# Performance work log

Hardware: AMD Instinct MI355X
Metric: run time of the kernel (lower is better)

## Reference

```python
import jax, jax.numpy as jnp
import numpy as np

B, N, D, H = 32, 64, 256, 256
WORD_NUM, REL_NUM, POS_NUM, CAT_NUM = 50000, 50, 48, 5


def setup_inputs() -> dict:
    key = jax.random.key(0)
    ks = jax.random.split(key, 20)
    rng = np.random.default_rng(0)
    # valid dependency trees: head[i] < i, head[0] = -1 (root)
    heads_np = np.zeros((B, N), dtype=np.int32)
    for b in range(B):
        heads_np[b, 0] = -1
        for i in range(1, N):
            heads_np[b, i] = rng.integers(0, i)
    p = lambda k, shape: (0.02 * jax.random.normal(k, shape)).astype(jnp.float32)
    z = lambda shape: jnp.zeros(shape, jnp.float32)
    return {
        "xs": jax.random.randint(ks[0], (B, N), 0, WORD_NUM),
        "heads": jnp.asarray(heads_np),
        "rels": jax.random.randint(ks[1], (B, N), 0, REL_NUM),
        "labels": jax.random.randint(ks[2], (B, N), 0, WORD_NUM),
        "poss": jax.random.randint(ks[3], (B, N), 0, POS_NUM),
        "xlengths": jnp.full((B,), N, dtype=jnp.int32),
        "target_start": jnp.zeros((B,), jnp.int32),
        "target_end": jnp.full((B,), N - 1, jnp.int32),
        "x_mask": jnp.ones((B, N), jnp.float32),
        # parameters
        "emb_W": p(ks[4], (WORD_NUM, D)),
        "rel_W": p(ks[5], (REL_NUM, D)),
        "gru_Wi_f": p(ks[6], (2 * D, 3 * H)), "gru_Wh_f": p(ks[7], (H, 3 * H)),
        "gru_bi_f": z((3 * H,)), "gru_bh_f": z((3 * H,)),
        "gru_Wi_b": p(ks[8], (2 * D, 3 * H)), "gru_Wh_b": p(ks[9], (H, 3 * H)),
        "gru_bi_b": z((3 * H,)), "gru_bh_b": z((3 * H,)),
        "Wt": p(ks[10], (2 * H, D)), "bt": z((D,)),
        "dt_Wx": p(ks[11], (2 * D, 3 * H)), "dt_Uh": p(ks[12], (H, 3 * H)), "dt_b": z((3 * H,)),
        "td_Wx": p(ks[13], (2 * D, 3 * H)), "td_Uh": p(ks[14], (H, 3 * H)), "td_b": z((3 * H,)),
        "fc_W": p(ks[15], (2 * H, 100)), "fc_b": z((100,)),
        "fc2_W": p(ks[16], (100, CAT_NUM)), "fc2_b": z((CAT_NUM,)),
    }


def _gru_cell(xpt, hprev, Uh, bh):
    gh = hprev @ Uh + bh
    xr, xz, xn = jnp.split(xpt, 3, axis=-1)
    hr, hz, hn = jnp.split(gh, 3, axis=-1)
    r = jax.nn.sigmoid(xr + hr)
    zg = jax.nn.sigmoid(xz + hz)
    n = jnp.tanh(xn + r * hn)
    return (1.0 - zg) * n + zg * hprev


def _gru_dir(x, Wi, Wh, bi, bh):
    # x: [B,N,2D] -> hidden sequence [B,N,H]
    xp = x @ Wi + bi  # precompute input projections
    def step(h, xpt):
        hnew = _gru_cell(xpt, h, Wh, bh)
        return hnew, hnew
    h0 = jnp.zeros((x.shape[0], Wh.shape[0]), x.dtype)
    _, hs = jax.lax.scan(step, h0, jnp.swapaxes(xp, 0, 1))
    return jnp.swapaxes(hs, 0, 1)


def _dt_tree(inputs, heads, Wx, Uh, b):
    # bottom-up (child-sum) tree GRU; heads[b,i] < i so reversed order is topological
    Bn, Nn, _ = inputs.shape
    Hh = Uh.shape[0]
    xp = inputs @ Wx + b
    bar = jnp.arange(Bn)
    def step(carry, idx):
        C, Hout = carry  # C: accumulated child hidden sums [B,N,H]
        h = _gru_cell(xp[:, idx], C[:, idx], Uh, jnp.zeros((3 * Hh,), inputs.dtype))
        Hout = Hout.at[:, idx].set(h)
        par = heads[:, idx]
        valid = par >= 0
        C = C.at[bar, jnp.where(valid, par, 0)].add(jnp.where(valid[:, None], h, 0.0))
        return (C, Hout), None
    H0 = jnp.zeros((Bn, Nn, Hh), inputs.dtype)
    (_, Hout), _ = jax.lax.scan(step, (H0, H0), jnp.arange(Nn - 1, -1, -1))
    return Hout


def _td_tree(inputs, heads, Wx, Uh, b):
    # top-down tree GRU: parent hidden flows to children; index order 0..N-1 is topological
    Bn, Nn, _ = inputs.shape
    Hh = Uh.shape[0]
    xp = inputs @ Wx + b
    bar = jnp.arange(Bn)
    def step(Hout, idx):
        par = heads[:, idx]
        valid = par >= 0
        hp = jnp.where(valid[:, None], Hout[bar, jnp.where(valid, par, 0)], 0.0)
        h = _gru_cell(xp[:, idx], hp, Uh, jnp.zeros((3 * Hh,), inputs.dtype))
        Hout = Hout.at[:, idx].set(h)
        return Hout, None
    H0 = jnp.zeros((Bn, Nn, Hh), inputs.dtype)
    Hout, _ = jax.lax.scan(step, H0, jnp.arange(Nn))
    return Hout


def reference(xs, heads, rels, labels, poss, xlengths, target_start, target_end, x_mask,
              emb_W, rel_W,
              gru_Wi_f, gru_Wh_f, gru_bi_f, gru_bh_f,
              gru_Wi_b, gru_Wh_b, gru_bi_b, gru_bh_b,
              Wt, bt, dt_Wx, dt_Uh, dt_b, td_Wx, td_Uh, td_b,
              fc_W, fc_b, fc2_W, fc2_b):
    word_emb = emb_W[xs]
    label_emb = emb_W[labels]  # original uses self.embedding for labels too
    emb = jnp.concatenate([word_emb, label_emb], axis=-1)  # [B,N,2D]
    fwd = _gru_dir(emb, gru_Wi_f, gru_Wh_f, gru_bi_f, gru_bh_f)
    bwd = jnp.flip(_gru_dir(jnp.flip(emb, 1), gru_Wi_b, gru_Wh_b, gru_bi_b, gru_bh_b), 1)
    grus = jnp.concatenate([fwd, bwd], axis=-1) @ Wt + bt  # transform -> [B,N,D]
    rel_emb = rel_W[rels]
    outputs = jnp.concatenate([grus, rel_emb], axis=-1)  # [B,N,2D]
    dt_out = _dt_tree(outputs, heads, dt_Wx, dt_Uh, dt_b)
    td_out = _td_tree(outputs, heads, td_Wx, td_Uh, td_b)
    ctx = jnp.concatenate([dt_out, td_out], axis=-1)  # [B,N,2H]
    ctx = jnp.max(ctx, axis=1)  # max_pool1d over length -> [B,2H]
    ctx = ctx @ fc_W + fc_b
    ctx = ctx @ fc2_W + fc2_b
    return ctx
```

## Files before the change

### kernel.cpp

```cpp
#include <hip/hip_runtime.h>


typedef _Float16 half2v __attribute__((ext_vector_type(2)));
typedef _Float16 half8 __attribute__((ext_vector_type(8)));
typedef unsigned int u32x32 __attribute__((ext_vector_type(32)));
typedef float f32x4v __attribute__((ext_vector_type(4)));

__device__ __forceinline__ float fdot2f(unsigned a, unsigned b, float c) {
#if __has_builtin(__builtin_amdgcn_fdot2)
  return __builtin_amdgcn_fdot2(__builtin_bit_cast(half2v, a),
                                __builtin_bit_cast(half2v, b), c, false);
#else
  half2v av = __builtin_bit_cast(half2v, a), bv = __builtin_bit_cast(half2v, b);
  return c + (float)av.x * (float)bv.x + (float)av.y * (float)bv.y;
#endif
}

__device__ __forceinline__ unsigned packh2(float x, float y) {
  half2v p;
  p.x = (_Float16)x;
  p.y = (_Float16)y;
  return __builtin_bit_cast(unsigned, p);
}
__device__ __forceinline__ float sigm(float x) { return 1.f / (1.f + __expf(-x)); }
__device__ __forceinline__ float tanh_fast(float x) {
  float cx = fminf(fmaxf(x, -15.f), 15.f);
  float e = __expf(2.f * cx);
  return (e - 1.f) / (e + 1.f);
}

__global__ __launch_bounds__(256) void pack_w(const float* __restrict__ W0,
                                              const float* __restrict__ W1,
                                              const float* __restrict__ W2,
                                              const float* __restrict__ W3, unsigned* P0,
                                              unsigned* P1, unsigned* P2, unsigned* P3) {
  const float* W;
  unsigned* P;
  switch (blockIdx.y) {
    case 0: W = W0; P = P0; break;
    case 1: W = W1; P = P1; break;
    case 2: W = W2; P = P2; break;
    default: W = W3; P = P3; break;
  }
  const int tid = blockIdx.x * 256 + threadIdx.x;
  const int i = tid & 3;
  const int u4 = tid >> 2;
  const int jg = u4 & 127;
  const int d4q = u4 >> 7;
  const int d4 = d4q % 48;
  const int q2 = d4q / 48;
  const int col2 = d4 / 24;
  const int rr = d4 % 24;
  const int g = rr >> 3;
  const int p4 = rr & 7;
  const int kp = p4 * 4 + i;
  const int k = q2 * 64 + kp * 2;
  const int col = g * 256 + col2 * 128 + jg;
  P[tid] = packh2(W[(size_t)k * 768 + col], W[(size_t)(k + 1) * 768 + col]);
}

template <int NP>
__device__ __forceinline__ void stage_w(const uint4* __restrict__ P4, int q2, int jg,
                                        int t, uint2 (*Wl)[512], u32x32& w0, u32x32& w1,
                                        u32x32& w2) {
#pragma unroll
  for (int p4 = 0; p4 < 8; ++p4) {
    uint4 v0 = P4[(q2 * 48 + p4) * 128 + jg];
    w0[4 * p4 + 0] = v0.x; w0[4 * p4 + 1] = v0.y;
    w0[4 * p4 + 2] = v0.z; w0[4 * p4 + 3] = v0.w;
    uint4 v1 = P4[(q2 * 48 + 8 + p4) * 128 + jg];
    w1[4 * p4 + 0] = v1.x; w1[4 * p4 + 1] = v1.y;
    w1[4 * p4 + 2] = v1.z; w1[4 * p4 + 3] = v1.w;
    uint4 v2 = P4[(q2 * 48 + 16 + p4) * 128 + jg];
    w2[4 * p4 + 0] = v2.x; w2[4 * p4 + 1] = v2.y;
    w2[4 * p4 + 2] = v2.z; w2[4 * p4 + 3] = v2.w;
  }
#pragma unroll
  for (int g = 0; g < 3; ++g)
#pragma unroll
    for (int p4 = 0; p4 < NP; ++p4) {
      uint4 v = P4[(q2 * 48 + 24 + g * 8 + p4) * 128 + jg];
      Wl[(g * NP + p4) * 2 + 0][t] = make_uint2(v.x, v.y);
      Wl[(g * NP + p4) * 2 + 1][t] = make_uint2(v.z, v.w);
    }
}

template <int NP>
__device__ __forceinline__ void dot_step(const u32x32& w0, const u32x32& w1,
                                         const u32x32& w2, const uint2 (*Wl)[512], int t,
                                         const uint4* __restrict__ P4, int sb,
                                         const uint4* hv4, float& a0, float& a1,
                                         float& a2, float& a3, float& a4, float& a5) {
#pragma unroll
  for (int c = 0; c < 8; ++c) {
    uint4 hu = hv4[c];
    a0 = fdot2f(w0[4 * c + 0], hu.x, a0); a0 = fdot2f(w0[4 * c + 1], hu.y, a0);
    a0 = fdot2f(w0[4 * c + 2], hu.z, a0); a0 = fdot2f(w0[4 * c + 3], hu.w, a0);
    a1 = fdot2f(w1[4 * c + 0], hu.x, a1); a1 = fdot2f(w1[4 * c + 1], hu.y, a1);
    a1 = fdot2f(w1[4 * c + 2], hu.z, a1); a1 = fdot2f(w1[4 * c + 3], hu.w, a1);
    a2 = fdot2f(w2[4 * c + 0], hu.x, a2); a2 = fdot2f(w2[4 * c + 1], hu.y, a2);
    a2 = fdot2f(w2[4 * c + 2], hu.z, a2); a2 = fdot2f(w2[4 * c + 3], hu.w, a2);
    if (c < NP) {
      uint2 u0 = Wl[(0 * NP + c) * 2 + 0][t], u1 = Wl[(0 * NP + c) * 2 + 1][t];
      a3 = fdot2f(u0.x, hu.x, a3); a3 = fdot2f(u0.y, hu.y, a3);
      a3 = fdot2f(u1.x, hu.z, a3); a3 = fdot2f(u1.y, hu.w, a3);
      uint2 v0 = Wl[(1 * NP + c) * 2 + 0][t], v1 = Wl[(1 * NP + c) * 2 + 1][t];
      a4 = fdot2f(v0.x, hu.x, a4); a4 = fdot2f(v0.y, hu.y, a4);
      a4 = fdot2f(v1.x, hu.z, a4); a4 = fdot2f(v1.y, hu.w, a4);
      uint2 x0 = Wl[(2 * NP + c) * 2 + 0][t], x1 = Wl[(2 * NP + c) * 2 + 1][t];
      a5 = fdot2f(x0.x, hu.x, a5); a5 = fdot2f(x0.y, hu.y, a5);
      a5 = fdot2f(x1.x, hu.z, a5); a5 = fdot2f(x1.y, hu.w, a5);
    } else {
      uint4 s0 = P4[sb + (0 * 8 + c) * 128];
      a3 = fdot2f(s0.x, hu.x, a3); a3 = fdot2f(s0.y, hu.y, a3);
      a3 = fdot2f(s0.z, hu.z, a3); a3 = fdot2f(s0.w, hu.w, a3);
      uint4 s1 = P4[sb + (1 * 8 + c) * 128];
      a4 = fdot2f(s1.x, hu.x, a4); a4 = fdot2f(s1.y, hu.y, a4);
      a4 = fdot2f(s1.z, hu.z, a4); a4 = fdot2f(s1.w, hu.w, a4);
      uint4 s2 = P4[sb + (2 * 8 + c) * 128];
      a5 = fdot2f(s2.x, hu.x, a5); a5 = fdot2f(s2.y, hu.y, a5);
      a5 = fdot2f(s2.z, hu.z, a5); a5 = fdot2f(s2.w, hu.w, a5);
    }
  }
}

__global__ void gather_emb(const int* __restrict__ xs, const int* __restrict__ labels,
                           const float* __restrict__ embW, float* __restrict__ emb) {
  const int row = blockIdx.x;
  const int t = threadIdx.x;
  const float4* W4 = (const float4*)embW;
  float4* dst = (float4*)(emb + (size_t)row * 512);
  if (t < 64)
    dst[t] = W4[(size_t)xs[row] * 64 + t];
  else
    dst[t] = W4[(size_t)labels[row] * 64 + (t - 64)];
}

__global__ void gather_rel(const int* __restrict__ rels, const float* __restrict__ relW,
                           float* __restrict__ outputs) {
  const int row = blockIdx.x;
  const int t = threadIdx.x;
  const float4* W4 = (const float4*)relW;
  float4* dst = (float4*)(outputs + (size_t)row * 512 + 256);
  dst[t] = W4[(size_t)rels[row] * 64 + t];
}

__global__ __launch_bounds__(256) void mm16s(const float* __restrict__ A,
                                             const float* __restrict__ W,
                                             const float* __restrict__ bias,
                                             float* __restrict__ C, int N, int ldc) {
  __shared__ __align__(16) _Float16 Ahi[64][40], Alo[64][40];
  __shared__ __align__(16) _Float16 Bhi[64][40], Blo[64][40];
  const int t = threadIdx.x, l = t & 63, w = t >> 6;
  const int bm = blockIdx.y * 64, bn = blockIdx.x * 64;
  const int ar = t >> 2, ac8 = (t & 3) * 8;
  const int bk = t >> 3, bn8 = (t & 7) * 8;
  f32x4v ac0 = {0.f, 0.f, 0.f, 0.f}, ac1 = ac0, ac2 = ac0, ac3 = ac0;
  const int fr = w * 16 + (l & 15), fc = (l >> 4) * 8, lo16 = l & 15;
  for (int kt = 0; kt < 512; kt += 32) {
    {
      const float* ap = A + (size_t)(bm + ar) * 512 + kt + ac8;
      float4 v0 = *(const float4*)ap;
      float4 v1 = *(const float4*)(ap + 4);
      float av[8] = {v0.x, v0.y, v0.z, v0.w, v1.x, v1.y, v1.z, v1.w};
#pragma unroll
      for (int i = 0; i < 8; ++i) {
        _Float16 h = (_Float16)av[i];
        Ahi[ar][ac8 + i] = h;
        Alo[ar][ac8 + i] = (_Float16)(av[i] - (float)h);
      }
    }
    {
      const float* wp = W + (size_t)(kt + bk) * N + bn + bn8;
      float4 v0 = *(const float4*)wp;
      float4 v1 = *(const float4*)(wp + 4);
      float wv[8] = {v0.x, v0.y, v0.z, v0.w, v1.x, v1.y, v1.z, v1.w};
#pragma unroll
      for (int i = 0; i < 8; ++i) {
        _Float16 h = (_Float16)wv[i];
        Bhi[bn8 + i][bk] = h;
        Blo[bn8 + i][bk] = (_Float16)(wv[i] - (float)h);
      }
    }
    __syncthreads();
    half8 avh = __builtin_bit_cast(half8, *(const uint4*)(&Ahi[fr][fc]));
    half8 avl = __builtin_bit_cast(half8, *(const uint4*)(&Alo[fr][fc]));
#define BH(NT) __builtin_bit_cast(half8, *(const uint4*)(&Bhi[(NT)*16 + lo16][fc]))
#define BL(NT) __builtin_bit_cast(half8, *(const uint4*)(&Blo[(NT)*16 + lo16][fc]))
    half8 b0h = BH(0), b1h = BH(1), b2h = BH(2), b3h = BH(3);
    half8 b0l = BL(0), b1l = BL(1), b2l = BL(2), b3l = BL(3);
#undef BH
#undef BL
    ac0 = __builtin_amdgcn_mfma_f32_16x16x32_f16(avh, b0h, ac0, 0, 0, 0);
    ac1 = __builtin_amdgcn_mfma_f32_16x16x32_f16(avh, b1h, ac1, 0, 0, 0);
    ac2 = __builtin_amdgcn_mfma_f32_16x16x32_f16(avh, b2h, ac2, 0, 0, 0);
    ac3 = __builtin_amdgcn_mfma_f32_16x16x32_f16(avh, b3h, ac3, 0, 0, 0);
    ac0 = __builtin_amdgcn_mfma_f32_16x16x32_f16(avh, b0l, ac0, 0, 0, 0);
    ac1 = __builtin_amdgcn_mfma_f32_16x16x32_f16(avh, b1l, ac1, 0, 0, 0);
    ac2 = __builtin_amdgcn_mfma_f32_16x16x32_f16(avh, b2l, ac2, 0, 0, 0);
    ac3 = __builtin_amdgcn_mfma_f32_16x16x32_f16(avh, b3l, ac3, 0, 0, 0);
    ac0 = __builtin_amdgcn_mfma_f32_16x16x32_f16(avl, b0h, ac0, 0, 0, 0);
    ac1 = __builtin_amdgcn_mfma_f32_16x16x32_f16(avl, b1h, ac1, 0, 0, 0);
    ac2 = __builtin_amdgcn_mfma_f32_16x16x32_f16(avl, b2h, ac2, 0, 0, 0);
    ac3 = __builtin_amdgcn_mfma_f32_16x16x32_f16(avl, b3h, ac3, 0, 0, 0);
    __syncthreads();
  }
  const int hi4 = l >> 4;
#define EPI(AC, NT)                                                            \
  {                                                                            \
    _Pragma("unroll") for (int i = 0; i < 4; ++i) {                            \
      const int row = bm + w * 16 + hi4 * 4 + i;                               \
      const int col = bn + (NT)*16 + lo16;                                     \
      C[(size_t)row * ldc + col] = (AC)[i] + bias[col];                        \
    }                                                                          \
  }
  EPI(ac0, 0) EPI(ac1, 1) EPI(ac2, 2) EPI(ac3, 3)
#undef EPI
}

__global__ __launch_bounds__(512) void gru_scan_h(
    const unsigned* __restrict__ Pf, const unsigned* __restrict__ Pb,
    const float* __restrict__ bh_f, const float* __restrict__ bh_b,
    const float* __restrict__ xp_f, const float* __restrict__ xp_b,
    float* __restrict__ grus) {
  const int b = blockIdx.x & 31, dir = blockIdx.x >> 5;
  const uint4* __restrict__ P4 = (const uint4*)(dir ? Pb : Pf);
  const float* __restrict__ bh = dir ? bh_b : bh_f;
  const float* __restrict__ xp = dir ? xp_b : xp_f;

  __shared__ uint2 Wl[36][512];
  __shared__ float part[4][3][256];
  __shared__ __align__(16) unsigned h2[128];

  const int t = threadIdx.x, jg = t & 127, q2 = t >> 7;
  const int sb = (q2 * 48 + 24) * 128 + jg;

  u32x32 w0, w1, w2;
  stage_w<6>(P4, q2, jg, t, Wl, w0, w1, w2);

  float br0 = 0.f, br1 = 0.f, bz0 = 0.f, bz1 = 0.f, bn0 = 0.f, bn1 = 0.f;
  float hp0 = 0.f, hp1 = 0.f;
  if (t < 128) {
    br0 = bh[2 * t];       br1 = bh[2 * t + 1];
    bz0 = bh[256 + 2 * t]; bz1 = bh[256 + 2 * t + 1];
    bn0 = bh[512 + 2 * t]; bn1 = bh[512 + 2 * t + 1];
    h2[t] = 0u;
  }
  __syncthreads();

  for (int s = 0; s < 64; ++s) {
    const int nn = dir ? (63 - s) : s;
    float2 pxr, pxz, pxn;
    if (t < 128) {
      const float* xrow = xp + (size_t)(b * 64 + nn) * 768;
      pxr = *(const float2*)(xrow + 2 * t);
      pxz = *(const float2*)(xrow + 256 + 2 * t);
      pxn = *(const float2*)(xrow + 512 + 2 * t);
    }
    float a0 = 0.f, a1 = 0.f, a2 = 0.f, a3 = 0.f, a4 = 0.f, a5 = 0.f;
    dot_step<6>(w0, w1, w2, Wl, t, P4, sb, (const uint4*)(h2 + q2 * 32), a0, a1, a2, a3,
                a4, a5);
    part[q2][0][jg] = a0;
    part[q2][0][128 + jg] = a3;
    part[q2][1][jg] = a1;
    part[q2][1][128 + jg] = a4;
    part[q2][2][jg] = a2;
    part[q2][2][128 + jg] = a5;
    __syncthreads();
    if (t < 128) {
      float s0r = 0, s1r = 0, s0z = 0, s1z = 0, s0n = 0, s1n = 0;
#pragma unroll
      for (int q = 0; q < 4; ++q) {
        float2 pr = *(const float2*)(&part[q][0][2 * t]); s0r += pr.x; s1r += pr.y;
        float2 pz = *(const float2*)(&part[q][1][2 * t]); s0z += pz.x; s1z += pz.y;
        float2 pn = *(const float2*)(&part[q][2][2 * t]); s0n += pn.x; s1n += pn.y;
      }
      float r0 = sigm(pxr.x + s0r + br0), r1 = sigm(pxr.y + s1r + br1);
      float z0 = sigm(pxz.x + s0z + bz0), z1 = sigm(pxz.y + s1z + bz1);
      float n0 = tanh_fast(pxn.x + r0 * (s0n + bn0));
      float n1 = tanh_fast(pxn.y + r1 * (s1n + bn1));
      float h0 = (1.f - z0) * n0 + z0 * hp0;
      float h1 = (1.f - z1) * n1 + z1 * hp1;
      hp0 = h0;
      hp1 = h1;
      h2[t] = packh2(h0, h1);
      float2 o;
      o.x = h0;
      o.y = h1;
      *(float2*)(grus + (size_t)(b * 64 + nn) * 512 + dir * 256 + 2 * t) = o;
    }
    __syncthreads();
  }
}

__global__ __launch_bounds__(512) void tree_scan_h(
    const unsigned* __restrict__ Pdt, const unsigned* __restrict__ Ptd,
    const float* __restrict__ xp_dt, const float* __restrict__ xp_td,
    const int* __restrict__ heads, float* __restrict__ ctx) {
  const int b = blockIdx.x & 31, istd = blockIdx.x >> 5;
  const uint4* __restrict__ P4 = (const uint4*)(istd ? Ptd : Pdt);
  const float* __restrict__ xp = istd ? xp_td : xp_dt;

  __shared__ float S[65][256];
  __shared__ __align__(16) unsigned S2[65][128];
  __shared__ uint2 Wl[12][512];
  __shared__ float part[4][3][256];
  __shared__ int hd[64];

  const int t = threadIdx.x, jg = t & 127, q2 = t >> 7;
  const int sb = (q2 * 48 + 24) * 128 + jg;

  u32x32 w0, w1, w2;
  stage_w<2>(P4, q2, jg, t, Wl, w0, w1, w2);

  for (int i = t; i < 65 * 256; i += 512) (&S[0][0])[i] = 0.f;
  for (int i = t; i < 65 * 128; i += 512) (&S2[0][0])[i] = 0u;
  if (t < 64) hd[t] = heads[b * 64 + t];
  __syncthreads();

  float mx0 = -1e30f, mx1 = -1e30f;

  for (int s = 0; s < 64; ++s) {
    const int idx = istd ? s : (63 - s);
    const int par = hd[idx];
    const int srow = istd ? (par >= 0 ? par : 64) : idx;

    float2 pxr, pxz, pxn;
    if (t < 128) {
      const float* xrow = xp + (size_t)(b * 64 + idx) * 768;
      pxr = *(const float2*)(xrow + 2 * t);
      pxz = *(const float2*)(xrow + 256 + 2 * t);
      pxn = *(const float2*)(xrow + 512 + 2 * t);
    }
    float a0 = 0.f, a1 = 0.f, a2 = 0.f, a3 = 0.f, a4 = 0.f, a5 = 0.f;
    dot_step<2>(w0, w1, w2, Wl, t, P4, sb, (const uint4*)(&S2[srow][q2 * 32]), a0, a1,
                a2, a3, a4, a5);
    part[q2][0][jg] = a0;
    part[q2][0][128 + jg] = a3;
    part[q2][1][jg] = a1;
    part[q2][1][128 + jg] = a4;
    part[q2][2][jg] = a2;
    part[q2][2][128 + jg] = a5;
    __syncthreads();
    if (t < 128) {
      float s0r = 0, s1r = 0, s0z = 0, s1z = 0, s0n = 0, s1n = 0;
#pragma unroll
      for (int q = 0; q < 4; ++q) {
        float2 pr = *(const float2*)(&part[q][0][2 * t]); s0r += pr.x; s1r += pr.y;
        float2 pz = *(const float2*)(&part[q][1][2 * t]); s0z += pz.x; s1z += pz.y;
        float2 pn = *(const float2*)(&part[q][2][2 * t]); s0n += pn.x; s1n += pn.y;
      }
      float r0 = sigm(pxr.x + s0r), r1 = sigm(pxr.y + s1r);
      float z0 = sigm(pxz.x + s0z), z1 = sigm(pxz.y + s1z);
      float n0 = tanh_fast(pxn.x + r0 * s0n), n1 = tanh_fast(pxn.y + r1 * s1n);
      float hp0 = S[srow][2 * t], hp1 = S[srow][2 * t + 1];
      float h0 = (1.f - z0) * n0 + z0 * hp0;
      float h1 = (1.f - z1) * n1 + z1 * hp1;
      mx0 = fmaxf(mx0, h0);
      mx1 = fmaxf(mx1, h1);
      if (istd) {
        S[idx][2 * t] = h0;
        S[idx][2 * t + 1] = h1;
        S2[idx][t] = packh2(h0, h1);
      } else if (par >= 0) {
        float c0 = S[par][2 * t] + h0;
        float c1 = S[par][2 * t + 1] + h1;
        S[par][2 * t] = c0;
        S[par][2 * t + 1] = c1;
        S2[par][t] = packh2(c0, c1);
      }
    }
    __syncthreads();
  }

  if (t < 128) {
    float2 o;
    o.x = mx0;
    o.y = mx1;
    *(float2*)(ctx + (size_t)b * 512 + istd * 256 + 2 * t) = o;
  }
}

__global__ __launch_bounds__(128) void final_k(const float* __restrict__ ctx_g,
                                               const float* __restrict__ fcW,
                                               const float* __restrict__ fcb,
                                               const float* __restrict__ fc2W,
                                               const float* __restrict__ fc2b,
                                               float* __restrict__ out) {
  const int b = blockIdx.x, t = threadIdx.x;
  __shared__ float ctx[512];
  __shared__ float f1[100];
  for (int i = t; i < 512; i += 128) ctx[i] = ctx_g[(size_t)b * 512 + i];
  __syncthreads();
  if (t < 100) {
    float a = fcb[t];
    for (int k = 0; k < 512; ++k) a = fmaf(ctx[k], fcW[k * 100 + t], a);
    f1[t] = a;
  }
  __syncthreads();
  if (t < 5) {
    float a = fc2b[t];
    for (int k = 0; k < 100; ++k) a = fmaf(f1[k], fc2W[k * 5 + t], a);
    out[b * 5 + t] = a;
  }
}

extern "C" void kernel_launch(void* const* d_in, const int* in_sizes, int n_in, void* d_out,
                              int out_size, void* d_ws, size_t ws_size, hipStream_t stream) {
  const int* xs = (const int*)d_in[0];
  const int* heads = (const int*)d_in[1];
  const int* rels = (const int*)d_in[2];
  const int* labels = (const int*)d_in[3];
  const float* emb_W = (const float*)d_in[9];
  const float* rel_W = (const float*)d_in[10];
  const float* Wi_f = (const float*)d_in[11];
  const float* Wh_f = (const float*)d_in[12];
  const float* bi_f = (const float*)d_in[13];
  const float* bh_f = (const float*)d_in[14];
  const float* Wi_b = (const float*)d_in[15];
  const float* Wh_b = (const float*)d_in[16];
  const float* bi_b = (const float*)d_in[17];
  const float* bh_b = (const float*)d_in[18];
  const float* Wt = (const float*)d_in[19];
  const float* bt = (const float*)d_in[20];
  const float* dt_Wx = (const float*)d_in[21];
  const float* dt_Uh = (const float*)d_in[22];
  const float* dt_b = (const float*)d_in[23];
  const float* td_Wx = (const float*)d_in[24];
  const float* td_Uh = (const float*)d_in[25];
  const float* td_b = (const float*)d_in[26];
  const float* fc_W = (const float*)d_in[27];
  const float* fc_b = (const float*)d_in[28];
  const float* fc2_W = (const float*)d_in[29];
  const float* fc2_b = (const float*)d_in[30];

  float* ws = (float*)d_ws;
  float* emb = ws;
  float* xp_f = ws + 1048576;
  float* xp_b = xp_f + 1572864;
  float* grus = xp_b + 1572864;
  float* ctx = grus + 1048576;
  unsigned* P0 = (unsigned*)(ctx + 16384);
  unsigned* P1 = P0 + 98304;
  unsigned* P2 = P1 + 98304;
  unsigned* P3 = P2 + 98304;
  float* outputs = emb;

  pack_w<<<dim3(384, 4), 256, 0, stream>>>(Wh_f, Wh_b, dt_Uh, td_Uh, P0, P1, P2, P3);
  gather_emb<<<2048, 128, 0, stream>>>(xs, labels, emb_W, emb);
  mm16s<<<dim3(12, 32), 256, 0, stream>>>(emb, Wi_f, bi_f, xp_f, 768, 768);
  mm16s<<<dim3(12, 32), 256, 0, stream>>>(emb, Wi_b, bi_b, xp_b, 768, 768);
  gru_scan_h<<<64, 512, 0, stream>>>(P0, P1, bh_f, bh_b, xp_f, xp_b, grus);
  mm16s<<<dim3(4, 32), 256, 0, stream>>>(grus, Wt, bt, outputs, 256, 512);
  gather_rel<<<2048, 64, 0, stream>>>(rels, rel_W, outputs);
  mm16s<<<dim3(12, 32), 256, 0, stream>>>(outputs, dt_Wx, dt_b, xp_f, 768, 768);
  mm16s<<<dim3(12, 32), 256, 0, stream>>>(outputs, td_Wx, td_b, xp_b, 768, 768);
  tree_scan_h<<<64, 512, 0, stream>>>(P2, P3, xp_f, xp_b, heads, ctx);
  final_k<<<32, 128, 0, stream>>>(ctx, fc_W, fc_b, fc2_W, fc2_b, (float*)d_out);
}
```

Baseline: 362.4 us.

## Pre-split operands into fp16 hi/lo with transposed weights for GEMMs

The fp16 hi/lo split used for the three-pass MFMA GEMMs now happens once, ahead of the GEMMs, instead of inside each k-tile. Embedding and rel gathers, and the Wt GEMM epilogue, write hi/lo fp16 activations directly. Input weights are transposed and split by a new tsplit kernel so the GEMM can load both operands as contiguous 16-byte vectors without per-element conversion or transposed LDS stores. This adds four small transpose launches and extra workspace traffic in exchange for cheaper GEMM inner loops.

```diff
diff --git a/kernel.cpp b/kernel.cpp
--- a/kernel.cpp
+++ b/kernel.cpp
@@ -21,6 +21,9 @@
   p.x = (_Float16)x;
   p.y = (_Float16)y;
   return __builtin_bit_cast(unsigned, p);
+}
+__device__ __forceinline__ unsigned short f2u(float x) {
+  return __builtin_bit_cast(unsigned short, (_Float16)x);
 }
 __device__ __forceinline__ float sigm(float x) { return 1.f / (1.f + __expf(-x)); }
 __device__ __forceinline__ float tanh_fast(float x) {
@@ -57,6 +60,225 @@
   const int k = q2 * 64 + kp * 2;
   const int col = g * 256 + col2 * 128 + jg;
   P[tid] = packh2(W[(size_t)k * 768 + col], W[(size_t)(k + 1) * 768 + col]);
+}
+
+__global__ __launch_bounds__(256) void tsplit(const float* __restrict__ W,
+                                              unsigned short* __restrict__ WThi,
+                                              unsigned short* __restrict__ WTlo, int K,
+                                              int N) {
+  __shared__ float T[32][33];
+  const int ky = blockIdx.y * 32, nx = blockIdx.x * 32;
+  const int r = threadIdx.x >> 3, c4 = (threadIdx.x & 7) * 4;
+  float4 v = *(const float4*)(W + (size_t)(ky + r) * N + nx + c4);
+  T[r][c4 + 0] = v.x;
+  T[r][c4 + 1] = v.y;
+  T[r][c4 + 2] = v.z;
+  T[r][c4 + 3] = v.w;
+  __syncthreads();
+  float f[4] = {T[c4 + 0][r], T[c4 + 1][r], T[c4 + 2][r], T[c4 + 3][r]};
+  ushort4 oh, ol;
+  {
+    _Float16 h0 = (_Float16)f[0], h1 = (_Float16)f[1], h2 = (_Float16)f[2],
+             h3 = (_Float16)f[3];
+    oh.x = __builtin_bit_cast(unsigned short, h0);
+    oh.y = __builtin_bit_cast(unsigned short, h1);
+    oh.z = __builtin_bit_cast(unsigned short, h2);
+    oh.w = __builtin_bit_cast(unsigned short, h3);
+    ol.x = f2u(f[0] - (float)h0);
+    ol.y = f2u(f[1] - (float)h1);
+    ol.z = f2u(f[2] - (float)h2);
+    ol.w = f2u(f[3] - (float)h3);
+  }
+  *(ushort4*)(WThi + (size_t)(nx + r) * K + ky + c4) = oh;
+  *(ushort4*)(WTlo + (size_t)(nx + r) * K + ky + c4) = ol;
+}
+
+__global__ void gather_emb_hl(const int* __restrict__ xs, const int* __restrict__ labels,
+                              const float* __restrict__ embW,
+                              unsigned short* __restrict__ eHi,
+                              unsigned short* __restrict__ eLo) {
+  const int row = blockIdx.x, t = threadIdx.x;
+  const float4* W4 = (const float4*)embW;
+  const int src = (t < 64) ? xs[row] : labels[row];
+  float4 v = W4[(size_t)src * 64 + (t & 63)];
+  float f[4] = {v.x, v.y, v.z, v.w};
+  ushort4 oh, ol;
+  _Float16 h0 = (_Float16)f[0], h1 = (_Float16)f[1], h2 = (_Float16)f[2],
+           h3 = (_Float16)f[3];
+  oh.x = __builtin_bit_cast(unsigned short, h0);
+  oh.y = __builtin_bit_cast(unsigned short, h1);
+  oh.z = __builtin_bit_cast(unsigned short, h2);
+  oh.w = __builtin_bit_cast(unsigned short, h3);
+  ol.x = f2u(f[0] - (float)h0);
+  ol.y = f2u(f[1] - (float)h1);
+  ol.z = f2u(f[2] - (float)h2);
+  ol.w = f2u(f[3] - (float)h3);
+  const size_t idx = (size_t)row * 512 + (t >> 6) * 256 + (t & 63) * 4;
+  *(ushort4*)(eHi + idx) = oh;
+  *(ushort4*)(eLo + idx) = ol;
+}
+
+__global__ void gather_rel_hl(const int* __restrict__ rels,
+                              const float* __restrict__ relW,
+                              unsigned short* __restrict__ oHi,
+                              unsigned short* __restrict__ oLo) {
+  const int row = blockIdx.x, t = threadIdx.x;
+  const float4* W4 = (const float4*)relW;
+  float4 v = W4[(size_t)rels[row] * 64 + t];
+  float f[4] = {v.x, v.y, v.z, v.w};
+  ushort4 oh, ol;
+  _Float16 h0 = (_Float16)f[0], h1 = (_Float16)f[1], h2 = (_Float16)f[2],
+           h3 = (_Float16)f[3];
+  oh.x = __builtin_bit_cast(unsigned short, h0);
+  oh.y = __builtin_bit_cast(unsigned short, h1);
+  oh.z = __builtin_bit_cast(unsigned short, h2);
+  oh.w = __builtin_bit_cast(unsigned short, h3);
+  ol.x = f2u(f[0] - (float)h0);
+  ol.y = f2u(f[1] - (float)h1);
+  ol.z = f2u(f[2] - (float)h2);
+  ol.w = f2u(f[3] - (float)h3);
+  const size_t idx = (size_t)row * 512 + 256 + t * 4;
+  *(ushort4*)(oHi + idx) = oh;
+  *(ushort4*)(oLo + idx) = ol;
+}
+
+__global__ __launch_bounds__(256) void mm16p(
+    const unsigned short* __restrict__ Ahi, const unsigned short* __restrict__ Alo,
+    const unsigned short* __restrict__ Bhi, const unsigned short* __restrict__ Blo,
+    const float* __restrict__ bias, float* __restrict__ Cf,
+    unsigned short* __restrict__ CHi, unsigned short* __restrict__ CLo, int ldc,
+    int mode) {
+  __shared__ __align__(16) _Float16 As_h[64][40], As_l[64][40];
+  __shared__ __align__(16) _Float16 Bs_h[64][40], Bs_l[64][40];
+  const int t = threadIdx.x, l = t & 63, w = t >> 6;
+  const int bm = blockIdx.y * 64, bn = blockIdx.x * 64;
+  const int sr = t >> 2, sc = (t & 3) * 8;
+  f32x4v ac0 = {0.f, 0.f, 0.f, 0.f}, ac1 = ac0, ac2 = ac0, ac3 = ac0;
+  const int fr = w * 16 + (l & 15), fc = (l >> 4) * 8, lo16 = l & 15;
+  for (int kt = 0; kt < 512; kt += 32) {
+    *(uint4*)(&As_h[sr][sc]) = *(const uint4*)(Ahi + (size_t)(bm + sr) * 512 + kt + sc);
+    *(uint4*)(&As_l[sr][sc]) = *(const uint4*)(Alo + (size_t)(bm + sr) * 512 + kt + sc);
+    *(uint4*)(&Bs_h[sr][sc]) = *(const uint4*)(Bhi + (size_t)(bn + sr) * 512 + kt + sc);
+    *(uint4*)(&Bs_l[sr][sc]) = *(const uint4*)(Blo + (size_t)(bn + sr) * 512 + kt + sc);
+    __syncthreads();
+    half8 avh = __builtin_bit_cast(half8, *(const uint4*)(&As_h[fr][fc]));
+    half8 avl = __builtin_bit_cast(half8, *(const uint4*)(&As_l[fr][fc]));
+#define BH(NT) __builtin_bit_cast(half8, *(const uint4*)(&Bs_h[(NT)*16 + lo16][fc]))
+#define BL(NT) __builtin_bit_cast(half8, *(const uint4*)(&Bs_l[(NT)*16 + lo16][fc]))
+    half8 b0h = BH(0), b1h = BH(1), b2h = BH(2), b3h = BH(3);
+    half8 b0l = BL(0), b1l = BL(1), b2l = BL(2), b3l = BL(3);
+#undef BH
+#undef BL
+    ac0 = __builtin_amdgcn_mfma_f32_16x16x32_f16(avh, b0h, ac0, 0, 0, 0);
+    ac1 = __builtin_amdgcn_mfma_f32_16x16x32_f16(avh, b1h, ac1, 0, 0, 0);
+    ac2 = __builtin_amdgcn_mfma_f32_16x16x32_f16(avh, b2h, ac2, 0, 0, 0);
+    ac3 = __builtin_amdgcn_mfma_f32_16x16x32_f16(avh, b3h, ac3, 0, 0, 0);
+    ac0 = __builtin_amdgcn_mfma_f32_16x16x32_f16(avh, b0l, ac0, 0, 0, 0);
+    ac1 = __builtin_amdgcn_mfma_f32_16x16x32_f16(avh, b1l, ac1, 0, 0, 0);
+    ac2 = __builtin_amdgcn_mfma_f32_16x16x32_f16(avh, b2l, ac2, 0, 0, 0);
+    ac3 = __builtin_amdgcn_mfma_f32_16x16x32_f16(avh, b3l, ac3, 0, 0, 0);
+    ac0 = __builtin_amdgcn_mfma_f32_16x16x32_f16(avl, b0h, ac0, 0, 0, 0);
+    ac1 = __builtin_amdgcn_mfma_f32_16x16x32_f16(avl, b1h, ac1, 0, 0, 0);
+    ac2 = __builtin_amdgcn_mfma_f32_16x16x32_f16(avl, b2h, ac2, 0, 0, 0);
+    ac3 = __builtin_amdgcn_mfma_f32_16x16x32_f16(avl, b3h, ac3, 0, 0, 0);
+    __syncthreads();
+  }
+  const int hi4 = l >> 4;
+#define EPI(AC, NT)                                                            \
+  {                                                                            \
+    _Pragma("unroll") for (int i = 0; i < 4; ++i) {                            \
+      const int row = bm + w * 16 + hi4 * 4 + i;                               \
+      const int col = bn + (NT)*16 + lo16;                                     \
+      float v = (AC)[i] + bias[col];                                           \
+      if (mode == 0) {                                                         \
+        Cf[(size_t)row * ldc + col] = v;                                       \
+      } else {                                                                 \
+        _Float16 h = (_Float16)v;                                              \
+        CHi[(size_t)row * ldc + col] = __builtin_bit_cast(unsigned short, h);  \
+        CLo[(size_t)row * ldc + col] = f2u(v - (float)h);                      \
+      }                                                                        \
+    }                                                                          \
+  }
+  EPI(ac0, 0) EPI(ac1, 1) EPI(ac2, 2) EPI(ac3, 3)
+#undef EPI
+}
+
+__global__ __launch_bounds__(256) void mm16s_wt(const float* __restrict__ A,
+                                                const float* __restrict__ W,
+                                                const float* __restrict__ bias,
+                                                unsigned short* __restrict__ CHi,
+                                                unsigned short* __restrict__ CLo, int N,
+                                                int ldc) {
+  __shared__ __align__(16) _Float16 Ahi[64][40], Alo[64][40];
+  __shared__ __align__(16) _Float16 Bhi[64][40], Blo[64][40];
+  const int t = threadIdx.x, l = t & 63, w = t >> 6;
+  const int bm = blockIdx.y * 64, bn = blockIdx.x * 64;
+  const int ar = t >> 2, ac8 = (t & 3) * 8;
+  const int bk = t >> 3, bn8 = (t & 7) * 8;
+  f32x4v ac0 = {0.f, 0.f, 0.f, 0.f}, ac1 = ac0, ac2 = ac0, ac3 = ac0;
+  const int fr = w * 16 + (l & 15), fc = (l >> 4) * 8, lo16 = l & 15;
+  for (int kt = 0; kt < 512; kt += 32) {
+    {
+      const float* ap = A + (size_t)(bm + ar) * 512 + kt + ac8;
+      float4 v0 = *(const float4*)ap;
+      float4 v1 = *(const float4*)(ap + 4);
+      float av[8] = {v0.x, v0.y, v0.z, v0.w, v1.x, v1.y, v1.z, v1.w};
+#pragma unroll
+      for (int i = 0; i < 8; ++i) {
+        _Float16 h = (_Float16)av[i];
+        Ahi[ar][ac8 + i] = h;
+        Alo[ar][ac8 + i] = (_Float16)(av[i] - (float)h);
+      }
+    }
+    {
+      const float* wp = W + (size_t)(kt + bk) * N + bn + bn8;
+      float4 v0 = *(const float4*)wp;
+      float4 v1 = *(const float4*)(wp + 4);
+      float wv[8] = {v0.x, v0.y, v0.z, v0.w, v1.x, v1.y, v1.z, v1.w};
+#pragma unroll
+      for (int i = 0; i < 8; ++i) {
+        _Float16 h = (_Float16)wv[i];
+        Bhi[bn8 + i][bk] = h;
+        Blo[bn8 + i][bk] = (_Float16)(wv[i] - (float)h);
+      }
+    }
+    __syncthreads();
+    half8 avh = __builtin_bit_cast(half8, *(const uint4*)(&Ahi[fr][fc]));
+    half8 avl = __builtin_bit_cast(half8, *(const uint4*)(&Alo[fr][fc]));
+#define BH(NT) __builtin_bit_cast(half8, *(const uint4*)(&Bhi[(NT)*16 + lo16][fc]))
+#define BL(NT) __builtin_bit_cast(half8, *(const uint4*)(&Blo[(NT)*16 + lo16][fc]))
+    half8 b0h = BH(0), b1h = BH(1), b2h = BH(2), b3h = BH(3);
+    half8 b0l = BL(0), b1l = BL(1), b2l = BL(2), b3l = BL(3);
+#undef BH
+#undef BL
+    ac0 = __builtin_amdgcn_mfma_f32_16x16x32_f16(avh, b0h, ac0, 0, 0, 0);
+    ac1 = __builtin_amdgcn_mfma_f32_16x16x32_f16(avh, b1h, ac1, 0, 0, 0);
+    ac2 = __builtin_amdgcn_mfma_f32_16x16x32_f16(avh, b2h, ac2, 0, 0, 0);
+    ac3 = __builtin_amdgcn_mfma_f32_16x16x32_f16(avh, b3h, ac3, 0, 0, 0);
+    ac0 = __builtin_amdgcn_mfma_f32_16x16x32_f16(avh, b0l, ac0, 0, 0, 0);
+    ac1 = __builtin_amdgcn_mfma_f32_16x16x32_f16(avh, b1l, ac1, 0, 0, 0);
+    ac2 = __builtin_amdgcn_mfma_f32_16x16x32_f16(avh, b2l, ac2, 0, 0, 0);
+    ac3 = __builtin_amdgcn_mfma_f32_16x16x32_f16(avh, b3l, ac3, 0, 0, 0);
+    ac0 = __builtin_amdgcn_mfma_f32_16x16x32_f16(avl, b0h, ac0, 0, 0, 0);
+    ac1 = __builtin_amdgcn_mfma_f32_16x16x32_f16(avl, b1h, ac1, 0, 0, 0);
+    ac2 = __builtin_amdgcn_mfma_f32_16x16x32_f16(avl, b2h, ac2, 0, 0, 0);
+    ac3 = __builtin_amdgcn_mfma_f32_16x16x32_f16(avl, b3h, ac3, 0, 0, 0);
+    __syncthreads();
+  }
+  const int hi4 = l >> 4;
+#define EPI(AC, NT)                                                            \
+  {                                                                            \
+    _Pragma("unroll") for (int i = 0; i < 4; ++i) {                            \
+      const int row = bm + w * 16 + hi4 * 4 + i;                               \
+      const int col = bn + (NT)*16 + lo16;                                     \
+      float v = (AC)[i] + bias[col];                                           \
+      _Float16 h = (_Float16)v;                                                \
+      CHi[(size_t)row * ldc + col] = __builtin_bit_cast(unsigned short, h);    \
+      CLo[(size_t)row * ldc + col] = f2u(v - (float)h);                        \
+    }                                                                          \
+  }
+  EPI(ac0, 0) EPI(ac1, 1) EPI(ac2, 2) EPI(ac3, 3)
+#undef EPI
 }
 
 template <int NP>
@@ -124,100 +346,6 @@
   }
 }
 
-__global__ void gather_emb(const int* __restrict__ xs, const int* __restrict__ labels,
-                           const float* __restrict__ embW, float* __restrict__ emb) {
-  const int row = blockIdx.x;
-  const int t = threadIdx.x;
-  const float4* W4 = (const float4*)embW;
-  float4* dst = (float4*)(emb + (size_t)row * 512);
-  if (t < 64)
-    dst[t] = W4[(size_t)xs[row] * 64 + t];
-  else
-    dst[t] = W4[(size_t)labels[row] * 64 + (t - 64)];
-}
-
-__global__ void gather_rel(const int* __restrict__ rels, const float* __restrict__ relW,
-                           float* __restrict__ outputs) {
-  const int row = blockIdx.x;
-  const int t = threadIdx.x;
-  const float4* W4 = (const float4*)relW;
-  float4* dst = (float4*)(outputs + (size_t)row * 512 + 256);
-  dst[t] = W4[(size_t)rels[row] * 64 + t];
-}
-
-__global__ __launch_bounds__(256) void mm16s(const float* __restrict__ A,
-                                             const float* __restrict__ W,
-                                             const float* __restrict__ bias,
-                                             float* __restrict__ C, int N, int ldc) {
-  __shared__ __align__(16) _Float16 Ahi[64][40], Alo[64][40];
-  __shared__ __align__(16) _Float16 Bhi[64][40], Blo[64][40];
-  const int t = threadIdx.x, l = t & 63, w = t >> 6;
-  const int bm = blockIdx.y * 64, bn = blockIdx.x * 64;
-  const int ar = t >> 2, ac8 = (t & 3) * 8;
-  const int bk = t >> 3, bn8 = (t & 7) * 8;
-  f32x4v ac0 = {0.f, 0.f, 0.f, 0.f}, ac1 = ac0, ac2 = ac0, ac3 = ac0;
-  const int fr = w * 16 + (l & 15), fc = (l >> 4) * 8, lo16 = l & 15;
-  for (int kt = 0; kt < 512; kt += 32) {
-    {
-      const float* ap = A + (size_t)(bm + ar) * 512 + kt + ac8;
-      float4 v0 = *(const float4*)ap;
-      float4 v1 = *(const float4*)(ap + 4);
-      float av[8] = {v0.x, v0.y, v0.z, v0.w, v1.x, v1.y, v1.z, v1.w};
-#pragma unroll
-      for (int i = 0; i < 8; ++i) {
-        _Float16 h = (_Float16)av[i];
-        Ahi[ar][ac8 + i] = h;
-        Alo[ar][ac8 + i] = (_Float16)(av[i] - (float)h);
-      }
-    }
-    {
-      const float* wp = W + (size_t)(kt + bk) * N + bn + bn8;
-      float4 v0 = *(const float4*)wp;
-      float4 v1 = *(const float4*)(wp + 4);
-      float wv[8] = {v0.x, v0.y, v0.z, v0.w, v1.x, v1.y, v1.z, v1.w};
-#pragma unroll
-      for (int i = 0; i < 8; ++i) {
-        _Float16 h = (_Float16)wv[i];
-        Bhi[bn8 + i][bk] = h;
-        Blo[bn8 + i][bk] = (_Float16)(wv[i] - (float)h);
-      }
-    }
-    __syncthreads();
-    half8 avh = __builtin_bit_cast(half8, *(const uint4*)(&Ahi[fr][fc]));
-    half8 avl = __builtin_bit_cast(half8, *(const uint4*)(&Alo[fr][fc]));
-#define BH(NT) __builtin_bit_cast(half8, *(const uint4*)(&Bhi[(NT)*16 + lo16][fc]))
-#define BL(NT) __builtin_bit_cast(half8, *(const uint4*)(&Blo[(NT)*16 + lo16][fc]))
-    half8 b0h = BH(0), b1h = BH(1), b2h = BH(2), b3h = BH(3);
-    half8 b0l = BL(0), b1l = BL(1), b2l = BL(2), b3l = BL(3);
-#undef BH
-#undef BL
-    ac0 = __builtin_amdgcn_mfma_f32_16x16x32_f16(avh, b0h, ac0, 0, 0, 0);
-    ac1 = __builtin_amdgcn_mfma_f32_16x16x32_f16(avh, b1h, ac1, 0, 0, 0);
-    ac2 = __builtin_amdgcn_mfma_f32_16x16x32_f16(avh, b2h, ac2, 0, 0, 0);
-    ac3 = __builtin_amdgcn_mfma_f32_16x16x32_f16(avh, b3h, ac3, 0, 0, 0);
-    ac0 = __builtin_amdgcn_mfma_f32_16x16x32_f16(avh, b0l, ac0, 0, 0, 0);
-    ac1 = __builtin_amdgcn_mfma_f32_16x16x32_f16(avh, b1l, ac1, 0, 0, 0);
-    ac2 = __builtin_amdgcn_mfma_f32_16x16x32_f16(avh, b2l, ac2, 0, 0, 0);
-    ac3 = __builtin_amdgcn_mfma_f32_16x16x32_f16(avh, b3l, ac3, 0, 0, 0);
-    ac0 = __builtin_amdgcn_mfma_f32_16x16x32_f16(avl, b0h, ac0, 0, 0, 0);
-    ac1 = __builtin_amdgcn_mfma_f32_16x16x32_f16(avl, b1h, ac1, 0, 0, 0);
-    ac2 = __builtin_amdgcn_mfma_f32_16x16x32_f16(avl, b2h, ac2, 0, 0, 0);
-    ac3 = __builtin_amdgcn_mfma_f32_16x16x32_f16(avl, b3h, ac3, 0, 0, 0);
-    __syncthreads();
-  }
-  const int hi4 = l >> 4;
-#define EPI(AC, NT)                                                            \
-  {                                                                            \
-    _Pragma("unroll") for (int i = 0; i < 4; ++i) {                            \
-      const int row = bm + w * 16 + hi4 * 4 + i;                               \
-      const int col = bn + (NT)*16 + lo16;                                     \
-      C[(size_t)row * ldc + col] = (AC)[i] + bias[col];                        \
-    }                                                                          \
-  }
-  EPI(ac0, 0) EPI(ac1, 1) EPI(ac2, 2) EPI(ac3, 3)
-#undef EPI
-}
-
 __global__ __launch_bounds__(512) void gru_scan_h(
     const unsigned* __restrict__ Pf, const unsigned* __restrict__ Pb,
     const float* __restrict__ bh_f, const float* __restrict__ bh_b,
@@ -435,26 +563,40 @@
   const float* fc2_b = (const float*)d_in[30];
 
   float* ws = (float*)d_ws;
-  float* emb = ws;
-  float* xp_f = ws + 1048576;
-  float* xp_b = xp_f + 1572864;
-  float* grus = xp_b + 1572864;
-  float* ctx = grus + 1048576;
-  unsigned* P0 = (unsigned*)(ctx + 16384);
+  float* xp_f = ws;
+  float* xp_b = ws + 1572864;
+  float* grus = ws + 3145728;
+  float* ctx = ws + 4194304;
+  unsigned* P0 = (unsigned*)(ws + 4210688);
   unsigned* P1 = P0 + 98304;
   unsigned* P2 = P1 + 98304;
   unsigned* P3 = P2 + 98304;
-  float* outputs = emb;
+  unsigned short* embHi = (unsigned short*)(ws + 4603904);
+  unsigned short* embLo = (unsigned short*)(ws + 5128192);
+  unsigned short* WTh_a = (unsigned short*)(ws + 5652480);
+  unsigned short* WTl_a = (unsigned short*)(ws + 5849088);
+  unsigned short* WTh_b = (unsigned short*)(ws + 6045696);
+  unsigned short* WTl_b = (unsigned short*)(ws + 6242304);
+  unsigned short* outHi = embHi;
+  unsigned short* outLo = embLo;
 
   pack_w<<<dim3(384, 4), 256, 0, stream>>>(Wh_f, Wh_b, dt_Uh, td_Uh, P0, P1, P2, P3);
-  gather_emb<<<2048, 128, 0, stream>>>(xs, labels, emb_W, emb);
-  mm16s<<<dim3(12, 32), 256, 0, stream>>>(emb, Wi_f, bi_f, xp_f, 768, 768);
-  mm16s<<<dim3(12, 32), 256, 0, stream>>>(emb, Wi_b, bi_b, xp_b, 768, 768);
+  tsplit<<<dim3(24, 16), 256, 0, stream>>>(Wi_f, WTh_a, WTl_a, 512, 768);
+  tsplit<<<dim3(24, 16), 256, 0, stream>>>(Wi_b, WTh_b, WTl_b, 512, 768);
+  gather_emb_hl<<<2048, 128, 0, stream>>>(xs, labels, emb_W, embHi, embLo);
+  mm16p<<<dim3(12, 32), 256, 0, stream>>>(embHi, embLo, WTh_a, WTl_a, bi_f, xp_f,
+                                          nullptr, nullptr, 768, 0);
+  mm16p<<<dim3(12, 32), 256, 0, stream>>>(embHi, embLo, WTh_b, WTl_b, bi_b, xp_b,
+                                          nullptr, nullptr, 768, 0);
   gru_scan_h<<<64, 512, 0, stream>>>(P0, P1, bh_f, bh_b, xp_f, xp_b, grus);
-  mm16s<<<dim3(4, 32), 256, 0, stream>>>(grus, Wt, bt, outputs, 256, 512);
-  gather_rel<<<2048, 64, 0, stream>>>(rels, rel_W, outputs);
-  mm16s<<<dim3(12, 32), 256, 0, stream>>>(outputs, dt_Wx, dt_b, xp_f, 768, 768);
-  mm16s<<<dim3(12, 32), 256, 0, stream>>>(outputs, td_Wx, td_b, xp_b, 768, 768);
+  tsplit<<<dim3(24, 16), 256, 0, stream>>>(dt_Wx, WTh_a, WTl_a, 512, 768);
+  tsplit<<<dim3(24, 16), 256, 0, stream>>>(td_Wx, WTh_b, WTl_b, 512, 768);
+  mm16s_wt<<<dim3(4, 32), 256, 0, stream>>>(grus, Wt, bt, outHi, outLo, 256, 512);
+  gather_rel_hl<<<2048, 64, 0, stream>>>(rels, rel_W, outHi, outLo);
+  mm16p<<<dim3(12, 32), 256, 0, stream>>>(outHi, outLo, WTh_a, WTl_a, dt_b, xp_f,
+                                          nullptr, nullptr, 768, 0);
+  mm16p<<<dim3(12, 32), 256, 0, stream>>>(outHi, outLo, WTh_b, WTl_b, td_b, xp_b,
+                                          nullptr, nullptr, 768, 0);
   tree_scan_h<<<64, 512, 0, stream>>>(P2, P3, xp_f, xp_b, heads, ctx);
   final_k<<<32, 128, 0, stream>>>(ctx, fc_W, fc_b, fc2_W, fc2_b, (float*)d_out);
 }
```

Result: faster. 328.0 us (-9.5%).
